# Optimization experiments

Measured on AMD Instinct MI355X. Metric: run time of the kernel, lower is better.

Reference implementation:

```python
import jax, jax.numpy as jnp
import numpy as np

C_IN = 128   # pair channel dim
H = 4        # heads
DH = 32      # per-head dim (c_hidden // no_heads = 128 // 4)
R = 96       # low-rank bias rank (hard-coded self.Rank)
N = 384      # sequence length (pair rep is N x N)
S_DIM = 449  # s_inputs feature dim (c_in + 449 into bias MLPs)
MLP_H = 256  # bias MLP hidden width
EPS = 1e-5


def setup_inputs() -> dict:
    key = jax.random.key(0)
    ks = jax.random.split(key, 16)
    w = lambda k, shp, s=0.02: (jax.random.normal(k, shp) * s).astype(jnp.float32)
    return {
        "x": jax.random.normal(ks[0], (N, N, C_IN), dtype=jnp.float32),
        "s_inputs": jax.random.normal(ks[1], (N, S_DIM), dtype=jnp.float32),
        "ln_gamma": jnp.ones((C_IN,), jnp.float32),
        "ln_beta": jnp.zeros((C_IN,), jnp.float32),
        # q flashbias MLP (Linear->Tanh->Linear->Tanh->Linear, no bias)
        "Wq1": w(ks[2], (C_IN + S_DIM, MLP_H)),
        "Wq2": w(ks[3], (MLP_H, MLP_H)),
        "Wq3": w(ks[4], (MLP_H, H * R)),
        # k flashbias MLP
        "Wk1": w(ks[5], (C_IN + S_DIM, MLP_H)),
        "Wk2": w(ks[6], (MLP_H, MLP_H)),
        "Wk3": w(ks[7], (MLP_H, H * R)),
        # OpenFold-style gated Attention params
        "Wq_att": w(ks[8], (C_IN, H * DH)),
        "Wk_att": w(ks[9], (C_IN, H * DH)),
        "Wv_att": w(ks[10], (C_IN, H * DH)),
        "Wg": w(ks[11], (C_IN, H * DH)),
        "bg": jnp.zeros((H * DH,), jnp.float32),
        "Wo": w(ks[12], (H * DH, C_IN)),
        "bo": jnp.zeros((C_IN,), jnp.float32),
        "id": 10,  # id < 16 -> low-rank flashbias path
    }


def _layer_norm(x, gamma, beta):
    mu = jnp.mean(x, axis=-1, keepdims=True)
    var = jnp.var(x, axis=-1, keepdims=True)
    return (x - mu) * jax.lax.rsqrt(var + EPS) * gamma + beta


def _bias_mlp(z, W1, W2, W3):
    # [N, C+449] -> [N, H*R] -> [1, H, N, R]
    h = jnp.tanh(jnp.tanh(z @ W1) @ W2) @ W3
    return jnp.transpose(h.reshape(N, H, R), (1, 0, 2))[None]


def reference(x, s_inputs, ln_gamma, ln_beta, Wq1, Wq2, Wq3, Wk1, Wk2, Wk3,
              Wq_att, Wk_att, Wv_att, Wg, bg, Wo, bo, id=10):
    # starting=True, eval mode, s_inputs given, id < 16 -> low-rank bias path
    x = _layer_norm(x, ln_gamma, ln_beta)                       # [N, N, C]

    # low-rank triangle-bias factors (shared across rows, broadcast over dim 0)
    q_bias = _bias_mlp(jnp.concatenate([x.mean(1), s_inputs], -1), Wq1, Wq2, Wq3)  # [1,H,N,R]
    k_bias = _bias_mlp(jnp.concatenate([x.mean(0), s_inputs], -1), Wk1, Wk2, Wk3)  # [1,H,N,R]

    # multi-head attention over the last sequence axis, per row
    def heads(z, W):  # [N, N, C] -> [N, H, N, DH]
        return jnp.transpose((z @ W).reshape(N, N, H, DH), (0, 2, 1, 3))

    q = heads(x, Wq_att) * (1.0 / np.sqrt(DH)).astype(np.float32)
    k = heads(x, Wk_att)
    v = heads(x, Wv_att)

    scores = jnp.einsum("ihqd,ihkd->ihqk", q, k)                # [N,H,N,N]
    scores = scores + jnp.einsum("bhqr,bhkr->bhqk", q_bias, k_bias)  # broadcast over rows
    a = jax.nn.softmax(scores, axis=-1)

    o = jnp.einsum("ihqk,ihkd->ihqd", a, v)                     # [N,H,N,DH]
    o = jnp.transpose(o, (0, 2, 1, 3)).reshape(N, N, H * DH)
    g = jax.nn.sigmoid(x @ Wg + bg)                              # gating
    out = (g * o) @ Wo + bo                                      # [N, N, C]
    return out
```

## Files before the change

kernel.cpp:

```cpp
#include <hip/hip_runtime.h>
#include <cstdint>
#include <cstddef>

typedef _Float16 f16;
typedef __attribute__((ext_vector_type(2))) _Float16 f16x2;
typedef __attribute__((ext_vector_type(4))) _Float16 f16x4;
typedef __attribute__((ext_vector_type(8))) _Float16 f16x8;
typedef __attribute__((ext_vector_type(4))) float f32x4;

#define MFMA_16x16x32(a,b,c) __builtin_amdgcn_mfma_f32_16x16x32_f16((a),(b),(c),0,0,0)
#define MFMA_16x16x16(a,b,c) __builtin_amdgcn_mfma_f32_16x16x16f16((a),(b),(c),0,0,0)

#define NSEQ 384
#define CIN 128
#define NH 4
#define DHD 32
#define RNK 96
#define SDIM 449
#define MHID 256
#define NN (NSEQ*NSEQ)

#define KPAD 608
#define ZSTR 616
#define HSTR 264
#define OFF_W1 0
#define SZ_W1 (MHID*KPAD)
#define OFF_W2 (2*SZ_W1)
#define SZ_W2 (MHID*MHID)
#define OFF_W3 (OFF_W2 + 2*SZ_W2)
#define SZ_W3 ((NH*RNK)*MHID)
#define WMLP_TOT (OFF_W3 + 2*SZ_W3)

__global__ __launch_bounds__(256) void k_convert(const float* __restrict__ Wq, const float* __restrict__ Wk,
    const float* __restrict__ Wv, const float* __restrict__ Wg, const float* __restrict__ Wo,
    f16* __restrict__ W4T, f16* __restrict__ WoT) {
  int idx = blockIdx.x*256 + threadIdx.x;
  int c = idx >> 7, kk = idx & 127;
  if (c < 512) {
    int mat = c >> 7, cc = c & 127;
    const float* src = mat==0 ? Wq : (mat==1 ? Wk : (mat==2 ? Wv : Wg));
    W4T[c*CIN + kk] = (f16)src[kk*CIN + cc];
  } else {
    int cc = c - 512;
    WoT[cc*CIN + kk] = (f16)Wo[kk*CIN + cc];
  }
}

__global__ __launch_bounds__(256) void k_convert2(const float* __restrict__ Wq1, const float* __restrict__ Wq2,
    const float* __restrict__ Wq3, const float* __restrict__ Wk1, const float* __restrict__ Wk2,
    const float* __restrict__ Wk3, f16* __restrict__ wmlp) {
  int idx = blockIdx.x*256 + threadIdx.x;
  float val;
  if (idx < OFF_W2) {
    int m = idx / SZ_W1, r = idx - m*SZ_W1;
    int c = r / KPAD, kk = r - c*KPAD;
    const float* src = m ? Wk1 : Wq1;
    val = (kk < SDIM + CIN) ? src[kk*MHID + c] : 0.f;
  } else if (idx < OFF_W3) {
    int r = idx - OFF_W2;
    int m = r >> 16, rr = r & 65535;
    int c = rr >> 8, kk = rr & 255;
    const float* src = m ? Wk2 : Wq2;
    val = src[kk*MHID + c];
  } else {
    int r = idx - OFF_W3;
    int m = r / SZ_W3, rr = r - m*SZ_W3;
    int c = rr >> 8, kk = rr & 255;
    const float* src = m ? Wk3 : Wq3;
    val = src[kk*(NH*RNK) + c];
  }
  wmlp[idx] = (f16)val;
}

__global__ __launch_bounds__(256) void k_ln(const float* __restrict__ x, const float* __restrict__ gamma,
    const float* __restrict__ beta, f16* __restrict__ xn, float* __restrict__ rowm) {
  int i = blockIdx.x; int t = threadIdx.x; int wave = t >> 6; int lane = t & 63;
  int c0 = lane*2;
  __shared__ float racc[CIN];
  if (t < CIN) racc[t] = 0.f;
  float g0 = gamma[c0], g1 = gamma[c0+1], be0 = beta[c0], be1 = beta[c0+1];
  float a0 = 0.f, a1 = 0.f;
  __syncthreads();
  for (int j = wave; j < NSEQ; j += 4) {
    const float2 v = *(const float2*)&x[(size_t)(i*NSEQ + j)*CIN + c0];
    float s = v.x + v.y, ss = v.x*v.x + v.y*v.y;
#pragma unroll
    for (int off = 32; off >= 1; off >>= 1) { s += __shfl_xor(s, off); ss += __shfl_xor(ss, off); }
    float mean = s * (1.0f/CIN);
    float var = ss * (1.0f/CIN) - mean*mean;
    float rs = rsqrtf(var + 1e-5f);
    float y0 = (v.x - mean)*rs*g0 + be0;
    float y1 = (v.y - mean)*rs*g1 + be1;
    f16x2 w; w[0] = (f16)y0; w[1] = (f16)y1;
    *(f16x2*)&xn[(size_t)(i*NSEQ + j)*CIN + c0] = w;
    a0 += y0; a1 += y1;
  }
  atomicAdd(&racc[c0], a0);
  atomicAdd(&racc[c0+1], a1);
  __syncthreads();
  if (t < CIN) rowm[i*CIN + t] = racc[t] * (1.0f/NSEQ);
}

__global__ __launch_bounds__(256) void k_colmean(const f16* __restrict__ xn, float* __restrict__ colm) {
  int j = blockIdx.x; int t = threadIdx.x;
  int c = t & 127, half = t >> 7;
  float acc = 0.f;
  int i0 = half*192;
#pragma unroll 4
  for (int ii = i0; ii < i0 + 192; ++ii)
    acc += (float)xn[(size_t)(ii*NSEQ + j)*CIN + c];
  __shared__ float sb[256];
  sb[t] = acc;
  __syncthreads();
  if (t < 128) colm[j*CIN + t] = (sb[t] + sb[t+128]) * (1.0f/NSEQ);
}

__global__ __launch_bounds__(256) void k_mlp2(const float* __restrict__ rowm, const float* __restrict__ colm,
    const float* __restrict__ sinp, const f16* __restrict__ wmlp,
    float* __restrict__ qbT, float* __restrict__ kbT) {
  int b = blockIdx.x;
  bool isQ = b < 12;
  int r0 = (isQ ? b : b - 12) * 32;
  const float* mean = isQ ? rowm : colm;
  const f16* W1T = wmlp + (isQ ? 0 : SZ_W1);
  const f16* W2T = wmlp + OFF_W2 + (isQ ? 0 : SZ_W2);
  const f16* W3T = wmlp + OFF_W3 + (isQ ? 0 : SZ_W3);
  float* outp = isQ ? qbT : kbT;
  int t = threadIdx.x, wave = t >> 6, lane = t & 63;
  int l15 = lane & 15, quad = lane >> 4;
  int rt = wave & 1, ch = wave >> 1;

  __shared__ __align__(16) f16 z[32*ZSTR];
  __shared__ __align__(16) f16 hbuf[2][32*HSTR];

  for (int idx = t; idx < 32*KPAD; idx += 256) {
    int row = idx / KPAD, u = idx - row*KPAD;
    float v;
    if (u < CIN) v = mean[(r0+row)*CIN + u];
    else if (u < CIN + SDIM) v = sinp[(r0+row)*SDIM + (u - CIN)];
    else v = 0.f;
    z[row*ZSTR + u] = (f16)v;
  }
  __syncthreads();

  {
    f32x4 acc[8];
#pragma unroll
    for (int c = 0; c < 8; ++c) acc[c] = (f32x4){0,0,0,0};
    for (int ks = 0; ks < 19; ++ks) {
      f16x8 af = *(const f16x8*)&z[(rt*16 + l15)*ZSTR + ks*32 + quad*8];
#pragma unroll
      for (int c = 0; c < 8; ++c) {
        f16x8 bf = *(const f16x8*)&W1T[(size_t)((ch*8 + c)*16 + l15)*KPAD + ks*32 + quad*8];
        acc[c] = MFMA_16x16x32(af, bf, acc[c]);
      }
    }
#pragma unroll
    for (int c = 0; c < 8; ++c) {
      int col = (ch*8 + c)*16 + l15;
#pragma unroll
      for (int r = 0; r < 4; ++r) {
        float th = 1.f - 2.f/(1.f + __expf(2.f*acc[c][r]));
        hbuf[0][(rt*16 + quad*4 + r)*HSTR + col] = (f16)th;
      }
    }
  }
  __syncthreads();

  {
    f32x4 acc[8];
#pragma unroll
    for (int c = 0; c < 8; ++c) acc[c] = (f32x4){0,0,0,0};
    for (int ks = 0; ks < 8; ++ks) {
      f16x8 af = *(const f16x8*)&hbuf[0][(rt*16 + l15)*HSTR + ks*32 + quad*8];
#pragma unroll
      for (int c = 0; c < 8; ++c) {
        f16x8 bf = *(const f16x8*)&W2T[(size_t)((ch*8 + c)*16 + l15)*MHID + ks*32 + quad*8];
        acc[c] = MFMA_16x16x32(af, bf, acc[c]);
      }
    }
#pragma unroll
    for (int c = 0; c < 8; ++c) {
      int col = (ch*8 + c)*16 + l15;
#pragma unroll
      for (int r = 0; r < 4; ++r) {
        float th = 1.f - 2.f/(1.f + __expf(2.f*acc[c][r]));
        hbuf[1][(rt*16 + quad*4 + r)*HSTR + col] = (f16)th;
      }
    }
  }
  __syncthreads();

  {
    f32x4 acc[12];
#pragma unroll
    for (int c = 0; c < 12; ++c) acc[c] = (f32x4){0,0,0,0};
    for (int ks = 0; ks < 8; ++ks) {
      f16x8 af = *(const f16x8*)&hbuf[1][(rt*16 + l15)*HSTR + ks*32 + quad*8];
#pragma unroll
      for (int c = 0; c < 12; ++c) {
        f16x8 bf = *(const f16x8*)&W3T[(size_t)((ch*12 + c)*16 + l15)*MHID + ks*32 + quad*8];
        acc[c] = MFMA_16x16x32(af, bf, acc[c]);
      }
    }
#pragma unroll
    for (int c = 0; c < 12; ++c) {
      int o = (ch*12 + c)*16 + l15;
#pragma unroll
      for (int r = 0; r < 4; ++r)
        outp[o*NSEQ + r0 + rt*16 + quad*4 + r] = acc[c][r];
    }
  }
}

__global__ __launch_bounds__(128) void k_bias(const float* __restrict__ qbT, const float* __restrict__ kbT,
    f16* __restrict__ biasT) {
  int b = blockIdx.x;
  int h = b / NSEQ, kk = b - h*NSEQ;
  int t = threadIdx.x;
  __shared__ float kr[RNK];
  if (t < RNK) kr[t] = kbT[(h*RNK + t)*NSEQ + kk];
  __syncthreads();
  float a0=0,a1=0,a2=0;
  for (int r = 0; r < RNK; ++r) {
    float kv = kr[r];
    const float* qrow = qbT + (h*RNK + r)*NSEQ;
    a0 += kv*qrow[t]; a1 += kv*qrow[t+128]; a2 += kv*qrow[t+256];
  }
  f16* dst = biasT + (size_t)(h*NSEQ + kk)*NSEQ;
  dst[t] = (f16)a0; dst[t+128] = (f16)a1; dst[t+256] = (f16)a2;
}

__global__ __launch_bounds__(256) void k_proj(const f16* __restrict__ xn, const f16* __restrict__ W4T,
    const float* __restrict__ bg, f16* __restrict__ qb, f16* __restrict__ kb, f16* __restrict__ vb,
    f16* __restrict__ gb) {
  int b = blockIdx.x; int mb = b >> 2, nb = b & 3;
  int t = threadIdx.x, wave = t >> 6, lane = t & 63;
  int l15 = lane & 15, quad = lane >> 4;
  __shared__ __align__(16) f16 As[128*128];
  __shared__ __align__(16) f16 Bs[128*128];
  int Mbase = mb*128;
  for (int p = 0; p < 8; ++p) {
    int c = p*256 + t; int row = c >> 4, ci = c & 15;
    int sw = (ci ^ (row & 15)) * 8;
    *(f16x8*)&As[row*128 + sw] = *(const f16x8*)&xn[(size_t)(Mbase + row)*CIN + ci*8];
    *(f16x8*)&Bs[row*128 + sw] = *(const f16x8*)&W4T[(size_t)(nb*128 + row)*CIN + ci*8];
  }
  __syncthreads();
  int m0 = wave*32;
  f16x8 af[2][4];
#pragma unroll
  for (int mt = 0; mt < 2; ++mt)
#pragma unroll
    for (int kt = 0; kt < 4; ++kt)
      af[mt][kt] = *(const f16x8*)&As[(m0 + mt*16 + l15)*128 + ((kt*4 + quad) ^ l15)*8];
  int i = mb/3, j0 = (mb - (mb/3)*3)*128 + m0;
#pragma unroll
  for (int ct = 0; ct < 8; ++ct) {
    f32x4 acc0 = (f32x4){0,0,0,0}, acc1 = (f32x4){0,0,0,0};
#pragma unroll
    for (int kt = 0; kt < 4; ++kt) {
      f16x8 bf = *(const f16x8*)&Bs[(ct*16 + l15)*128 + ((kt*4 + quad) ^ l15)*8];
      acc0 = MFMA_16x16x32(af[0][kt], bf, acc0);
      acc1 = MFMA_16x16x32(af[1][kt], bf, acc1);
    }
    int col = nb*128 + ct*16 + l15;
    int cc = col & 127;
    int hh = cc >> 5, d = cc & 31;
    if (nb == 3) {
      float bgv = bg[cc];
#pragma unroll
      for (int mt = 0; mt < 2; ++mt) {
        f32x4 a = mt ? acc1 : acc0;
#pragma unroll
        for (int r = 0; r < 4; ++r) {
          int jj = j0 + mt*16 + quad*4 + r;
          float sg = 1.0f/(1.0f + __expf(-(a[r] + bgv)));
          gb[(size_t)(i*NSEQ + jj)*CIN + cc] = (f16)sg;
        }
      }
    } else {
      f16* dstb = nb==0 ? qb : (nb==1 ? kb : vb);
      float scale = nb==0 ? 0.17677669529663687f : 1.0f;
#pragma unroll
      for (int mt = 0; mt < 2; ++mt) {
        f32x4 a = mt ? acc1 : acc0;
#pragma unroll
        for (int r = 0; r < 4; ++r) {
          int jj = j0 + mt*16 + quad*4 + r;
          dstb[((size_t)(i*NH + hh)*NSEQ + jj)*DHD + d] = (f16)(a[r]*scale);
        }
      }
    }
  }
}

__global__ __launch_bounds__(256) void k_attn(const f16* __restrict__ qg, const f16* __restrict__ kg,
    const f16* __restrict__ vg, const f16* __restrict__ biasT, f16* __restrict__ og) {
  int b = blockIdx.x; int h = b & 3; int i = b >> 2;
  int t = threadIdx.x; int wave = t >> 6; int lane = t & 63;
  int l15 = lane & 15, quad = lane >> 4;
  __shared__ __align__(16) f16 Ks[NSEQ*40];
  __shared__ __align__(16) f16 Vs[NSEQ*36];
  size_t base = (size_t)(i*NH + h) * NSEQ * DHD;
  for (int p = 0; p < 6; ++p) {
    int c = p*256 + t; int row = c >> 2, ci = c & 3;
    *(f16x8*)&Ks[row*40 + ci*8] = *(const f16x8*)&kg[base + row*DHD + ci*8];
  }
  for (int p = 0; p < 12; ++p) {
    int c = p*256 + t; int row = c >> 3, ci = c & 7;
    *(f16x4*)&Vs[row*36 + ci*4] = *(const f16x4*)&vg[base + row*DHD + ci*4];
  }
  int qt0 = wave*6;
  f16x8 qf[6];
#pragma unroll
  for (int s = 0; s < 6; ++s)
    qf[s] = *(const f16x8*)&qg[base + (size_t)((qt0+s)*16 + l15)*DHD + quad*8];
  f32x4 oa[6][2];
  float lsum[6];
#pragma unroll
  for (int s = 0; s < 6; ++s) { lsum[s] = 0.f; oa[s][0] = (f32x4){0,0,0,0}; oa[s][1] = (f32x4){0,0,0,0}; }
  __syncthreads();
  const f16* bb = biasT + (size_t)h*NSEQ*NSEQ;
  for (int kt = 0; kt < 24; ++kt) {
    f16x8 kf = *(const f16x8*)&Ks[(kt*16 + l15)*40 + quad*8];
    int vbase = (kt*16 + quad*4)*36 + l15;
    f16x4 vf0, vf1;
#pragma unroll
    for (int jj = 0; jj < 4; ++jj) { vf0[jj] = Vs[vbase + jj*36]; vf1[jj] = Vs[vbase + jj*36 + 16]; }
    const f16* bp = bb + (size_t)(kt*16 + quad*4)*NSEQ + l15;
    f32x4 cb[6];
#pragma unroll
    for (int s = 0; s < 6; ++s) {
      int qc = (qt0 + s)*16;
      cb[s][0] = (float)bp[qc];
      cb[s][1] = (float)bp[qc + NSEQ];
      cb[s][2] = (float)bp[qc + 2*NSEQ];
      cb[s][3] = (float)bp[qc + 3*NSEQ];
    }
#pragma unroll
    for (int s = 0; s < 6; ++s) {
      f32x4 st = MFMA_16x16x32(kf, qf[s], cb[s]);
      float p0 = __expf(st[0]), p1 = __expf(st[1]), p2 = __expf(st[2]), p3 = __expf(st[3]);
      lsum[s] += (p0 + p1) + (p2 + p3);
      f16x4 pa; pa[0]=(f16)p0; pa[1]=(f16)p1; pa[2]=(f16)p2; pa[3]=(f16)p3;
      oa[s][0] = MFMA_16x16x16(pa, vf0, oa[s][0]);
      oa[s][1] = MFMA_16x16x16(pa, vf1, oa[s][1]);
    }
  }
#pragma unroll
  for (int s = 0; s < 6; ++s) {
    float lf = lsum[s];
    lf += __shfl_xor(lf, 16);
    lf += __shfl_xor(lf, 32);
    float inv = 1.0f / lf;
#pragma unroll
    for (int r = 0; r < 4; ++r) {
      float invr = __shfl(inv, quad*4 + r);
      int qrow = (qt0+s)*16 + quad*4 + r;
      size_t ob = (size_t)(i*NSEQ + qrow)*(NH*DHD) + h*DHD;
      og[ob + l15]      = (f16)(oa[s][0][r] * invr);
      og[ob + 16 + l15] = (f16)(oa[s][1][r] * invr);
    }
  }
}

__global__ __launch_bounds__(256) void k_final(const f16* __restrict__ gb, const f16* __restrict__ ob,
    const f16* __restrict__ WoT, const float* __restrict__ bo, float* __restrict__ out) {
  int mb = blockIdx.x;
  int t = threadIdx.x, wave = t >> 6, lane = t & 63;
  int l15 = lane & 15, quad = lane >> 4;
  __shared__ __align__(16) f16 As[128*128];
  __shared__ __align__(16) f16 Bs[128*128];
  int Mbase = mb*128;
  for (int p = 0; p < 8; ++p) {
    int c = p*256 + t; int row = c >> 4, ci = c & 15;
    int sw = (ci ^ (row & 15)) * 8;
    f16x8 gv = *(const f16x8*)&gb[(size_t)(Mbase + row)*CIN + ci*8];
    f16x8 ov = *(const f16x8*)&ob[(size_t)(Mbase + row)*CIN + ci*8];
    *(f16x8*)&As[row*128 + sw] = gv*ov;
    *(f16x8*)&Bs[row*128 + sw] = *(const f16x8*)&WoT[row*CIN + ci*8];
  }
  __syncthreads();
  int m0 = wave*32;
  f16x8 af[2][4];
#pragma unroll
  for (int mt = 0; mt < 2; ++mt)
#pragma unroll
    for (int kt = 0; kt < 4; ++kt)
      af[mt][kt] = *(const f16x8*)&As[(m0 + mt*16 + l15)*128 + ((kt*4 + quad) ^ l15)*8];
#pragma unroll
  for (int ct = 0; ct < 8; ++ct) {
    f32x4 acc0 = (f32x4){0,0,0,0}, acc1 = (f32x4){0,0,0,0};
#pragma unroll
    for (int kt = 0; kt < 4; ++kt) {
      f16x8 bf = *(const f16x8*)&Bs[(ct*16 + l15)*128 + ((kt*4 + quad) ^ l15)*8];
      acc0 = MFMA_16x16x32(af[0][kt], bf, acc0);
      acc1 = MFMA_16x16x32(af[1][kt], bf, acc1);
    }
    float bov = bo[ct*16 + l15];
#pragma unroll
    for (int mt = 0; mt < 2; ++mt) {
      f32x4 a = mt ? acc1 : acc0;
#pragma unroll
      for (int r = 0; r < 4; ++r) {
        int mrow = Mbase + m0 + mt*16 + quad*4 + r;
        out[(size_t)mrow*CIN + ct*16 + l15] = a[r] + bov;
      }
    }
  }
}

extern "C" void kernel_launch(void* const* d_in, const int* in_sizes, int n_in,
                              void* d_out, int out_size, void* d_ws, size_t ws_size,
                              hipStream_t stream) {
  (void)in_sizes; (void)n_in; (void)out_size; (void)ws_size;
  const float* x    = (const float*)d_in[0];
  const float* sinp = (const float*)d_in[1];
  const float* gam  = (const float*)d_in[2];
  const float* bet  = (const float*)d_in[3];
  const float* Wq1  = (const float*)d_in[4];
  const float* Wq2  = (const float*)d_in[5];
  const float* Wq3  = (const float*)d_in[6];
  const float* Wk1  = (const float*)d_in[7];
  const float* Wk2  = (const float*)d_in[8];
  const float* Wk3  = (const float*)d_in[9];
  const float* Wqa  = (const float*)d_in[10];
  const float* Wka  = (const float*)d_in[11];
  const float* Wva  = (const float*)d_in[12];
  const float* Wg   = (const float*)d_in[13];
  const float* bg   = (const float*)d_in[14];
  const float* Wo   = (const float*)d_in[15];
  const float* bo   = (const float*)d_in[16];
  float* out = (float*)d_out;

  char* w = (char*)d_ws;
  auto carve = [&](size_t bytes) { char* p = w; w += (bytes + 255) & ~(size_t)255; return p; };
  f16*   xn    = (f16*)carve((size_t)NN*CIN*2);
  f16*   qb    = (f16*)carve((size_t)NN*CIN*2);
  f16*   kb    = (f16*)carve((size_t)NN*CIN*2);
  f16*   vb    = (f16*)carve((size_t)NN*CIN*2);
  f16*   gbuf  = (f16*)carve((size_t)NN*CIN*2);
  f16*   biasT = (f16*)carve((size_t)NH*NSEQ*NSEQ*2);
  float* rowm  = (float*)carve((size_t)NSEQ*CIN*4);
  float* colm  = (float*)carve((size_t)NSEQ*CIN*4);
  float* qbT   = (float*)carve((size_t)(NH*RNK)*NSEQ*4);
  float* kbT   = (float*)carve((size_t)(NH*RNK)*NSEQ*4);
  f16*   W4T   = (f16*)carve((size_t)512*CIN*2);
  f16*   WoT   = (f16*)carve((size_t)CIN*CIN*2);
  f16*   wmlp  = (f16*)carve((size_t)WMLP_TOT*2);
  f16*   obuf  = xn;

  k_convert<<<320, 256, 0, stream>>>(Wqa, Wka, Wva, Wg, Wo, W4T, WoT);
  k_convert2<<<WMLP_TOT/256, 256, 0, stream>>>(Wq1, Wq2, Wq3, Wk1, Wk2, Wk3, wmlp);
  k_ln<<<NSEQ, 256, 0, stream>>>(x, gam, bet, xn, rowm);
  k_colmean<<<NSEQ, 256, 0, stream>>>(xn, colm);
  k_mlp2<<<24, 256, 0, stream>>>(rowm, colm, sinp, wmlp, qbT, kbT);
  k_bias<<<NH*NSEQ, 128, 0, stream>>>(qbT, kbT, biasT);
  k_proj<<<4608, 256, 0, stream>>>(xn, W4T, bg, qb, kb, vb, gbuf);
  k_attn<<<NH*NSEQ, 256, 0, stream>>>(qb, kb, vb, biasT, obuf);
  k_final<<<1152, 256, 0, stream>>>(gbuf, obuf, WoT, bo, out);
}
```

Measured before the change: 522.4 us.

## Store bias in MFMA-fragment fp32 layout and widen layernorm grid

The low-rank bias matrix is now written in fp32, laid out so each attention lane loads its 4-element MFMA accumulator fragment with one 16-byte vector load. Before, each lane made four scattered fp16 gathers per tile. The layernorm kernel now splits each row across four blocks with float4 loads, giving more parallelism. Row means are accumulated with global atomics into a buffer that is zeroed first. The cost is double the bias memory footprint and nondeterministic float atomics in the row mean.

```diff
diff --git a/kernel.cpp b/kernel.cpp
--- a/kernel.cpp
+++ b/kernel.cpp
@@ -74,31 +74,39 @@
 
 __global__ __launch_bounds__(256) void k_ln(const float* __restrict__ x, const float* __restrict__ gamma,
     const float* __restrict__ beta, f16* __restrict__ xn, float* __restrict__ rowm) {
-  int i = blockIdx.x; int t = threadIdx.x; int wave = t >> 6; int lane = t & 63;
-  int c0 = lane*2;
+  int b = blockIdx.x;
+  int i = b >> 2, jbase = (b & 3) * 96;
+  int t = threadIdx.x, wave = t >> 6, lane = t & 63;
+  int half = lane >> 5, l31 = lane & 31;
+  int c0 = l31 * 4;
   __shared__ float racc[CIN];
   if (t < CIN) racc[t] = 0.f;
-  float g0 = gamma[c0], g1 = gamma[c0+1], be0 = beta[c0], be1 = beta[c0+1];
-  float a0 = 0.f, a1 = 0.f;
-  __syncthreads();
-  for (int j = wave; j < NSEQ; j += 4) {
-    const float2 v = *(const float2*)&x[(size_t)(i*NSEQ + j)*CIN + c0];
-    float s = v.x + v.y, ss = v.x*v.x + v.y*v.y;
-#pragma unroll
-    for (int off = 32; off >= 1; off >>= 1) { s += __shfl_xor(s, off); ss += __shfl_xor(ss, off); }
+  float4 g4 = *(const float4*)&gamma[c0];
+  float4 b4 = *(const float4*)&beta[c0];
+  float a0=0,a1=0,a2=0,a3=0;
+  __syncthreads();
+  for (int it = 0; it < 12; ++it) {
+    int j = jbase + it*8 + wave*2 + half;
+    const float4 v = *(const float4*)&x[(size_t)(i*NSEQ + j)*CIN + c0];
+    float s = (v.x+v.y)+(v.z+v.w);
+    float ss = (v.x*v.x+v.y*v.y)+(v.z*v.z+v.w*v.w);
+#pragma unroll
+    for (int off = 16; off >= 1; off >>= 1) { s += __shfl_xor(s, off); ss += __shfl_xor(ss, off); }
     float mean = s * (1.0f/CIN);
     float var = ss * (1.0f/CIN) - mean*mean;
     float rs = rsqrtf(var + 1e-5f);
-    float y0 = (v.x - mean)*rs*g0 + be0;
-    float y1 = (v.y - mean)*rs*g1 + be1;
-    f16x2 w; w[0] = (f16)y0; w[1] = (f16)y1;
-    *(f16x2*)&xn[(size_t)(i*NSEQ + j)*CIN + c0] = w;
-    a0 += y0; a1 += y1;
-  }
-  atomicAdd(&racc[c0], a0);
-  atomicAdd(&racc[c0+1], a1);
-  __syncthreads();
-  if (t < CIN) rowm[i*CIN + t] = racc[t] * (1.0f/NSEQ);
+    float y0 = (v.x-mean)*rs*g4.x + b4.x;
+    float y1 = (v.y-mean)*rs*g4.y + b4.y;
+    float y2 = (v.z-mean)*rs*g4.z + b4.z;
+    float y3 = (v.w-mean)*rs*g4.w + b4.w;
+    f16x4 w; w[0]=(f16)y0; w[1]=(f16)y1; w[2]=(f16)y2; w[3]=(f16)y3;
+    *(f16x4*)&xn[(size_t)(i*NSEQ + j)*CIN + c0] = w;
+    a0+=y0; a1+=y1; a2+=y2; a3+=y3;
+  }
+  atomicAdd(&racc[c0], a0); atomicAdd(&racc[c0+1], a1);
+  atomicAdd(&racc[c0+2], a2); atomicAdd(&racc[c0+3], a3);
+  __syncthreads();
+  if (t < CIN) atomicAdd(&rowm[i*CIN + t], racc[t] * (1.0f/NSEQ));
 }
 
 __global__ __launch_bounds__(256) void k_colmean(const f16* __restrict__ xn, float* __restrict__ colm) {
@@ -214,21 +222,32 @@
 }
 
 __global__ __launch_bounds__(128) void k_bias(const float* __restrict__ qbT, const float* __restrict__ kbT,
-    f16* __restrict__ biasT) {
+    float* __restrict__ bias4) {
   int b = blockIdx.x;
-  int h = b / NSEQ, kk = b - h*NSEQ;
+  int h = b / 96, kg = b - h*96;
   int t = threadIdx.x;
-  __shared__ float kr[RNK];
-  if (t < RNK) kr[t] = kbT[(h*RNK + t)*NSEQ + kk];
-  __syncthreads();
-  float a0=0,a1=0,a2=0;
+  __shared__ float4 kr[RNK];
+  if (t < RNK) kr[t] = *(const float4*)&kbT[(size_t)(h*RNK + t)*NSEQ + kg*4];
+  __syncthreads();
+  float acc[3][4];
+#pragma unroll
+  for (int m = 0; m < 3; ++m)
+#pragma unroll
+    for (int r = 0; r < 4; ++r) acc[m][r] = 0.f;
   for (int r = 0; r < RNK; ++r) {
-    float kv = kr[r];
-    const float* qrow = qbT + (h*RNK + r)*NSEQ;
-    a0 += kv*qrow[t]; a1 += kv*qrow[t+128]; a2 += kv*qrow[t+256];
-  }
-  f16* dst = biasT + (size_t)(h*NSEQ + kk)*NSEQ;
-  dst[t] = (f16)a0; dst[t+128] = (f16)a1; dst[t+256] = (f16)a2;
+    float4 kv = kr[r];
+    const float* qrow = qbT + (size_t)(h*RNK + r)*NSEQ;
+    float q0 = qrow[t], q1 = qrow[t+128], q2 = qrow[t+256];
+    acc[0][0]+=q0*kv.x; acc[0][1]+=q0*kv.y; acc[0][2]+=q0*kv.z; acc[0][3]+=q0*kv.w;
+    acc[1][0]+=q1*kv.x; acc[1][1]+=q1*kv.y; acc[1][2]+=q1*kv.z; acc[1][3]+=q1*kv.w;
+    acc[2][0]+=q2*kv.x; acc[2][1]+=q2*kv.y; acc[2][2]+=q2*kv.z; acc[2][3]+=q2*kv.w;
+  }
+#pragma unroll
+  for (int m = 0; m < 3; ++m) {
+    int q = t + m*128;
+    f32x4 w; w[0]=acc[m][0]; w[1]=acc[m][1]; w[2]=acc[m][2]; w[3]=acc[m][3];
+    *(f32x4*)&bias4[((size_t)b*NSEQ + q)*4] = w;
+  }
 }
 
 __global__ __launch_bounds__(256) void k_proj(const f16* __restrict__ xn, const f16* __restrict__ W4T,
@@ -296,7 +315,7 @@
 }
 
 __global__ __launch_bounds__(256) void k_attn(const f16* __restrict__ qg, const f16* __restrict__ kg,
-    const f16* __restrict__ vg, const f16* __restrict__ biasT, f16* __restrict__ og) {
+    const f16* __restrict__ vg, const float* __restrict__ bias4, f16* __restrict__ og) {
   int b = blockIdx.x; int h = b & 3; int i = b >> 2;
   int t = threadIdx.x; int wave = t >> 6; int lane = t & 63;
   int l15 = lane & 15, quad = lane >> 4;
@@ -321,23 +340,16 @@
 #pragma unroll
   for (int s = 0; s < 6; ++s) { lsum[s] = 0.f; oa[s][0] = (f32x4){0,0,0,0}; oa[s][1] = (f32x4){0,0,0,0}; }
   __syncthreads();
-  const f16* bb = biasT + (size_t)h*NSEQ*NSEQ;
   for (int kt = 0; kt < 24; ++kt) {
     f16x8 kf = *(const f16x8*)&Ks[(kt*16 + l15)*40 + quad*8];
     int vbase = (kt*16 + quad*4)*36 + l15;
     f16x4 vf0, vf1;
 #pragma unroll
     for (int jj = 0; jj < 4; ++jj) { vf0[jj] = Vs[vbase + jj*36]; vf1[jj] = Vs[vbase + jj*36 + 16]; }
-    const f16* bp = bb + (size_t)(kt*16 + quad*4)*NSEQ + l15;
+    const float* bp = bias4 + (((size_t)h*96 + kt*4 + quad)*NSEQ + qt0*16 + l15)*4;
     f32x4 cb[6];
 #pragma unroll
-    for (int s = 0; s < 6; ++s) {
-      int qc = (qt0 + s)*16;
-      cb[s][0] = (float)bp[qc];
-      cb[s][1] = (float)bp[qc + NSEQ];
-      cb[s][2] = (float)bp[qc + 2*NSEQ];
-      cb[s][3] = (float)bp[qc + 3*NSEQ];
-    }
+    for (int s = 0; s < 6; ++s) cb[s] = *(const f32x4*)(bp + s*64);
 #pragma unroll
     for (int s = 0; s < 6; ++s) {
       f32x4 st = MFMA_16x16x32(kf, qf[s], cb[s]);
@@ -441,7 +453,7 @@
   f16*   kb    = (f16*)carve((size_t)NN*CIN*2);
   f16*   vb    = (f16*)carve((size_t)NN*CIN*2);
   f16*   gbuf  = (f16*)carve((size_t)NN*CIN*2);
-  f16*   biasT = (f16*)carve((size_t)NH*NSEQ*NSEQ*2);
+  float* bias4 = (float*)carve((size_t)NH*NSEQ*NSEQ*4);
   float* rowm  = (float*)carve((size_t)NSEQ*CIN*4);
   float* colm  = (float*)carve((size_t)NSEQ*CIN*4);
   float* qbT   = (float*)carve((size_t)(NH*RNK)*NSEQ*4);
@@ -451,13 +463,14 @@
   f16*   wmlp  = (f16*)carve((size_t)WMLP_TOT*2);
   f16*   obuf  = xn;
 
+  hipMemsetAsync(rowm, 0, (size_t)NSEQ*CIN*4, stream);
   k_convert<<<320, 256, 0, stream>>>(Wqa, Wka, Wva, Wg, Wo, W4T, WoT);
   k_convert2<<<WMLP_TOT/256, 256, 0, stream>>>(Wq1, Wq2, Wq3, Wk1, Wk2, Wk3, wmlp);
-  k_ln<<<NSEQ, 256, 0, stream>>>(x, gam, bet, xn, rowm);
+  k_ln<<<NSEQ*4, 256, 0, stream>>>(x, gam, bet, xn, rowm);
   k_colmean<<<NSEQ, 256, 0, stream>>>(xn, colm);
   k_mlp2<<<24, 256, 0, stream>>>(rowm, colm, sinp, wmlp, qbT, kbT);
-  k_bias<<<NH*NSEQ, 128, 0, stream>>>(qbT, kbT, biasT);
+  k_bias<<<NH*96, 128, 0, stream>>>(qbT, kbT, bias4);
   k_proj<<<4608, 256, 0, stream>>>(xn, W4T, bg, qb, kb, vb, gbuf);
-  k_attn<<<NH*NSEQ, 256, 0, stream>>>(qb, kb, vb, biasT, obuf);
+  k_attn<<<NH*NSEQ, 256, 0, stream>>>(qb, kb, vb, bias4, obuf);
   k_final<<<1152, 256, 0, stream>>>(gbuf, obuf, WoT, bo, out);
 }
```

New measurement: 458.5 us. 1.14x faster.
